# Performance work log

Measured on AMD Instinct MI355X. Metric: run time of the kernel, lower is better.

The kernel has to match this reference:

```python
import jax, jax.numpy as jnp
import numpy as np

N_NODES = 50000


def _gcn_norm(edge_index, edge_weight, num_nodes):
    """Add self-loops (weight 1) and compute symmetric GCN normalization.
    Returns (src, dst, norm) over the augmented edge set."""
    src = jnp.concatenate([edge_index[0], jnp.arange(num_nodes, dtype=edge_index.dtype)])
    dst = jnp.concatenate([edge_index[1], jnp.arange(num_nodes, dtype=edge_index.dtype)])
    w = jnp.concatenate([edge_weight, jnp.ones((num_nodes,), dtype=edge_weight.dtype)])
    deg = jax.ops.segment_sum(w, dst, num_segments=num_nodes)  # [N]
    deg_inv_sqrt = jnp.where(deg > 0, jax.lax.rsqrt(jnp.where(deg > 0, deg, 1.0)), 0.0)
    norm = deg_inv_sqrt[src] * w * deg_inv_sqrt[dst]  # [E+N]
    return src, dst, norm


def _gcn_conv(x, W, b, src, dst, norm, num_nodes):
    h = x @ W                                   # [N, out] linear first (PyG order)
    msg = h[src] * norm[:, None]                # [E+N, out] gather + scale
    out = jax.ops.segment_sum(msg, dst, num_segments=num_nodes)  # scatter-add
    return out + b


def setup_inputs() -> dict:
    key = jax.random.key(0)
    ks = jax.random.split(key, 9)
    N, E = N_NODES, 800000
    x = jax.random.normal(ks[0], (N, 256), dtype=jnp.float32)
    edge_index = jax.random.randint(ks[1], (2, E), 0, N, dtype=jnp.int64)
    edge_attr = jax.random.uniform(ks[2], (E,), dtype=jnp.float32)
    W1 = jax.random.normal(ks[3], (256, 128), dtype=jnp.float32) * (1.0 / np.sqrt(256))
    b1 = jnp.zeros((128,), dtype=jnp.float32)
    W2 = jax.random.normal(ks[4], (128, 128), dtype=jnp.float32) * (1.0 / np.sqrt(128))
    b2 = jnp.zeros((128,), dtype=jnp.float32)
    W3 = jax.random.normal(ks[5], (128, 128), dtype=jnp.float32) * (1.0 / np.sqrt(128))
    b3 = jnp.zeros((128,), dtype=jnp.float32)
    return {"x": x, "edge_index": edge_index, "edge_attr": edge_attr,
            "W1": W1, "b1": b1, "W2": W2, "b2": b2, "W3": W3, "b3": b3}


def reference(x, edge_index, edge_attr, W1, b1, W2, b2, W3, b3):
    N = x.shape[0]
    src, dst, norm = _gcn_norm(edge_index, edge_attr, N)
    x1 = jax.nn.relu(_gcn_conv(x, W1, b1, src, dst, norm, N))
    x2 = jax.nn.relu(_gcn_conv(x1, W2, b2, src, dst, norm, N))
    return jax.nn.relu(_gcn_conv(x2, W3, b3, src, dst, norm, N))
```

## Files before the change

kernel.cpp:

```cpp
#include <hip/hip_runtime.h>
#include <math.h>

#define F_OUT 128
#define MAXDEG 64

typedef __attribute__((ext_vector_type(8))) short short8v;
typedef __attribute__((ext_vector_type(4))) float f32x4;
typedef unsigned long long ull;

__device__ inline ushort f2bf(float x) {
    uint u = __float_as_uint(x);
    uint r = (u + 0x7FFFu + ((u >> 16) & 1u)) >> 16;
    return (ushort)r;
}
__device__ inline float bf2f(ushort h) { return __uint_as_float((uint)h << 16); }
__device__ inline uint pack2(ushort a, ushort b) { return (uint)a | ((uint)b << 16); }

__device__ inline float slot_sumw(ull s) {
    return (float)((double)(s & ((1ull << 40) - 1)) * (1.0 / 8388608.0));
}


__global__ __launch_bounds__(128) void prep_kernel(const float* __restrict__ W1,
                                                   ushort* W1th, ushort* W1tl,
                                                   ull* slot, int n) {
    int b = blockIdx.x;
    if (b < 256) {
        int idx = b * 128 + threadIdx.x;
        int k = idx >> 7, c = idx & 127;
        float x = W1[idx];
        ushort h = f2bf(x);
        ushort l = f2bf(x - bf2f(h));
        W1th[(size_t)c * 256 + k] = h;
        W1tl[(size_t)c * 256 + k] = l;
    } else {
        int i = (b - 256) * 128 + threadIdx.x;
        if (i < n) slot[i] = 0ull;
    }
}


__device__ __forceinline__ void fill_edge(const int* __restrict__ src,
                                          const int* __restrict__ dst,
                                          const float* __restrict__ w,
                                          ull* slot, int2* es, int e) {
    int s = src[e], d = dst[e];
    float wv = w[e];
    ull inc = (1ull << 40) | (ull)(uint)(wv * 8388608.0f + 0.5f);
    ull old = atomicAdd(&slot[d], inc);
    uint pos = (uint)(old >> 40);
    if (pos < MAXDEG) es[(size_t)d * MAXDEG + pos] = make_int2(s, __float_as_int(wv));
}

__global__ void coef_kernel(int2* es, const ull* __restrict__ slot, int n) {
    int i = blockIdx.x * blockDim.x + threadIdx.x;
    if (i < n * MAXDEG) {
        int d = i >> 6;
        int pos = i & (MAXDEG - 1);
        int cnt = (int)(slot[d] >> 40);
        if (pos < cnt) {
            int2 e = es[i];
            float dsrc = rsqrtf(1.0f + slot_sumw(slot[e.x]));
            es[i].y = __float_as_int(dsrc * __int_as_float(e.y));
        }
    }
}


template <int K>
__device__ __forceinline__ void gemm_body(ushort* sAh, ushort* sAl,
                                          ushort* sBh, ushort* sBl,
                                          const float* __restrict__ in,
                                          const ushort* __restrict__ Wth,
                                          const ushort* __restrict__ Wtl,
                                          ushort* __restrict__ hbf, int n, int bb) {
    const int t = threadIdx.x;
    const int lane = t & 63;
    const int wv = t >> 6;
    const int block_row = bb * 64;

    const int arow = t >> 1;
    const int ahalf = t & 1;
    const int bcol = t;

    const int l15 = lane & 15;
    const int koct = lane >> 4;

    f32x4 acc[4][4];
    #pragma unroll
    for (int r = 0; r < 4; ++r)
        #pragma unroll
        for (int c = 0; c < 4; ++c) acc[r][c] = (f32x4){0.f, 0.f, 0.f, 0.f};

    const int grow_a = block_row + arow;
    const bool arow_ok = grow_a < n;

    for (int kt = 0; kt < K / 32; ++kt) {
        const int k0 = kt * 32;

        {
            float v[16];
            if (arow_ok) {
                const float4* p = reinterpret_cast<const float4*>(
                    &in[(size_t)grow_a * K + k0 + ahalf * 16]);
                float4 f0 = p[0], f1 = p[1], f2 = p[2], f3 = p[3];
                v[0]=f0.x; v[1]=f0.y; v[2]=f0.z; v[3]=f0.w;
                v[4]=f1.x; v[5]=f1.y; v[6]=f1.z; v[7]=f1.w;
                v[8]=f2.x; v[9]=f2.y; v[10]=f2.z; v[11]=f2.w;
                v[12]=f3.x; v[13]=f3.y; v[14]=f3.z; v[15]=f3.w;
            } else {
                #pragma unroll
                for (int i = 0; i < 16; ++i) v[i] = 0.f;
            }
            ushort hh[16], ll[16];
            #pragma unroll
            for (int i = 0; i < 16; ++i) {
                hh[i] = f2bf(v[i]);
                ll[i] = f2bf(v[i] - bf2f(hh[i]));
            }
            const int c0 = 2 * ahalf, c1 = 2 * ahalf + 1;
            *reinterpret_cast<uint4*>(&sAh[(c0 * 64 + arow) * 8]) =
                make_uint4(pack2(hh[0],hh[1]), pack2(hh[2],hh[3]), pack2(hh[4],hh[5]), pack2(hh[6],hh[7]));
            *reinterpret_cast<uint4*>(&sAh[(c1 * 64 + arow) * 8]) =
                make_uint4(pack2(hh[8],hh[9]), pack2(hh[10],hh[11]), pack2(hh[12],hh[13]), pack2(hh[14],hh[15]));
            *reinterpret_cast<uint4*>(&sAl[(c0 * 64 + arow) * 8]) =
                make_uint4(pack2(ll[0],ll[1]), pack2(ll[2],ll[3]), pack2(ll[4],ll[5]), pack2(ll[6],ll[7]));
            *reinterpret_cast<uint4*>(&sAl[(c1 * 64 + arow) * 8]) =
                make_uint4(pack2(ll[8],ll[9]), pack2(ll[10],ll[11]), pack2(ll[12],ll[13]), pack2(ll[14],ll[15]));
        }
        {
            const uint4* ph = reinterpret_cast<const uint4*>(&Wth[(size_t)bcol * K + k0]);
            const uint4* pl = reinterpret_cast<const uint4*>(&Wtl[(size_t)bcol * K + k0]);
            #pragma unroll
            for (int j = 0; j < 4; ++j)
                *reinterpret_cast<uint4*>(&sBh[(j * 128 + bcol) * 8]) = ph[j];
            #pragma unroll
            for (int j = 0; j < 4; ++j)
                *reinterpret_cast<uint4*>(&sBl[(j * 128 + bcol) * 8]) = pl[j];
        }
        __syncthreads();

        short8v a_h[4], a_l[4], b_h[4], b_l[4];
        #pragma unroll
        for (int r = 0; r < 4; ++r) {
            a_h[r] = *reinterpret_cast<const short8v*>(&sAh[(koct * 64 + r * 16 + l15) * 8]);
            a_l[r] = *reinterpret_cast<const short8v*>(&sAl[(koct * 64 + r * 16 + l15) * 8]);
        }
        #pragma unroll
        for (int c = 0; c < 4; ++c) {
            b_h[c] = *reinterpret_cast<const short8v*>(&sBh[(koct * 128 + wv * 64 + c * 16 + l15) * 8]);
            b_l[c] = *reinterpret_cast<const short8v*>(&sBl[(koct * 128 + wv * 64 + c * 16 + l15) * 8]);
        }
        #pragma unroll
        for (int r = 0; r < 4; ++r)
            #pragma unroll
            for (int c = 0; c < 4; ++c) {
                acc[r][c] = __builtin_amdgcn_mfma_f32_16x16x32_bf16(a_h[r], b_h[c], acc[r][c], 0, 0, 0);
                acc[r][c] = __builtin_amdgcn_mfma_f32_16x16x32_bf16(a_h[r], b_l[c], acc[r][c], 0, 0, 0);
                acc[r][c] = __builtin_amdgcn_mfma_f32_16x16x32_bf16(a_l[r], b_h[c], acc[r][c], 0, 0, 0);
            }
        __syncthreads();
    }

    #pragma unroll
    for (int r = 0; r < 4; ++r) {
        #pragma unroll
        for (int c = 0; c < 4; ++c) {
            int gcol = wv * 64 + c * 16 + l15;
            #pragma unroll
            for (int j = 0; j < 4; ++j) {
                int grow = block_row + r * 16 + koct * 4 + j;
                if (grow < n) hbf[(size_t)grow * F_OUT + gcol] = f2bf(acc[r][c][j]);
            }
        }
    }
}


template <int K>
__global__ __launch_bounds__(128) void gemm_presplit(const ushort* __restrict__ ahp,
                                                     const ushort* __restrict__ alp,
                                                     const ushort* __restrict__ Wth,
                                                     const ushort* __restrict__ Wtl,
                                                     ushort* __restrict__ hbf, int n) {
    __shared__ ushort sAh[64 * 32], sAl[64 * 32];
    __shared__ ushort sBh[128 * 32], sBl[128 * 32];

    const int t = threadIdx.x;
    const int lane = t & 63;
    const int wv = t >> 6;
    const int block_row = blockIdx.x * 64;

    const int arow = t >> 1;
    const int ahalf = t & 1;
    const int bcol = t;

    const int l15 = lane & 15;
    const int koct = lane >> 4;

    f32x4 acc[4][4];
    #pragma unroll
    for (int r = 0; r < 4; ++r)
        #pragma unroll
        for (int c = 0; c < 4; ++c) acc[r][c] = (f32x4){0.f, 0.f, 0.f, 0.f};

    const int grow_a = block_row + arow;
    const bool arow_ok = grow_a < n;
    const uint4 zero4 = make_uint4(0u, 0u, 0u, 0u);

    for (int kt = 0; kt < K / 32; ++kt) {
        const int k0 = kt * 32;
        const int c0 = 2 * ahalf, c1 = 2 * ahalf + 1;

        if (arow_ok) {
            const uint4* ph = reinterpret_cast<const uint4*>(&ahp[(size_t)grow_a * K + k0 + ahalf * 16]);
            const uint4* pl = reinterpret_cast<const uint4*>(&alp[(size_t)grow_a * K + k0 + ahalf * 16]);
            *reinterpret_cast<uint4*>(&sAh[(c0 * 64 + arow) * 8]) = ph[0];
            *reinterpret_cast<uint4*>(&sAh[(c1 * 64 + arow) * 8]) = ph[1];
            *reinterpret_cast<uint4*>(&sAl[(c0 * 64 + arow) * 8]) = pl[0];
            *reinterpret_cast<uint4*>(&sAl[(c1 * 64 + arow) * 8]) = pl[1];
        } else {
            *reinterpret_cast<uint4*>(&sAh[(c0 * 64 + arow) * 8]) = zero4;
            *reinterpret_cast<uint4*>(&sAh[(c1 * 64 + arow) * 8]) = zero4;
            *reinterpret_cast<uint4*>(&sAl[(c0 * 64 + arow) * 8]) = zero4;
            *reinterpret_cast<uint4*>(&sAl[(c1 * 64 + arow) * 8]) = zero4;
        }
        {
            const uint4* ph = reinterpret_cast<const uint4*>(&Wth[(size_t)bcol * K + k0]);
            const uint4* pl = reinterpret_cast<const uint4*>(&Wtl[(size_t)bcol * K + k0]);
            #pragma unroll
            for (int j = 0; j < 4; ++j)
                *reinterpret_cast<uint4*>(&sBh[(j * 128 + bcol) * 8]) = ph[j];
            #pragma unroll
            for (int j = 0; j < 4; ++j)
                *reinterpret_cast<uint4*>(&sBl[(j * 128 + bcol) * 8]) = pl[j];
        }
        __syncthreads();

        short8v a_h[4], a_l[4], b_h[4], b_l[4];
        #pragma unroll
        for (int r = 0; r < 4; ++r) {
            a_h[r] = *reinterpret_cast<const short8v*>(&sAh[(koct * 64 + r * 16 + l15) * 8]);
            a_l[r] = *reinterpret_cast<const short8v*>(&sAl[(koct * 64 + r * 16 + l15) * 8]);
        }
        #pragma unroll
        for (int c = 0; c < 4; ++c) {
            b_h[c] = *reinterpret_cast<const short8v*>(&sBh[(koct * 128 + wv * 64 + c * 16 + l15) * 8]);
            b_l[c] = *reinterpret_cast<const short8v*>(&sBl[(koct * 128 + wv * 64 + c * 16 + l15) * 8]);
        }
        #pragma unroll
        for (int r = 0; r < 4; ++r)
            #pragma unroll
            for (int c = 0; c < 4; ++c) {
                acc[r][c] = __builtin_amdgcn_mfma_f32_16x16x32_bf16(a_h[r], b_h[c], acc[r][c], 0, 0, 0);
                acc[r][c] = __builtin_amdgcn_mfma_f32_16x16x32_bf16(a_h[r], b_l[c], acc[r][c], 0, 0, 0);
                acc[r][c] = __builtin_amdgcn_mfma_f32_16x16x32_bf16(a_l[r], b_h[c], acc[r][c], 0, 0, 0);
            }
        __syncthreads();
    }

    #pragma unroll
    for (int r = 0; r < 4; ++r) {
        #pragma unroll
        for (int c = 0; c < 4; ++c) {
            int gcol = wv * 64 + c * 16 + l15;
            #pragma unroll
            for (int j = 0; j < 4; ++j) {
                int grow = block_row + r * 16 + koct * 4 + j;
                if (grow < n) hbf[(size_t)grow * F_OUT + gcol] = f2bf(acc[r][c][j]);
            }
        }
    }
}


__global__ __launch_bounds__(128) void mega1_kernel(
        const float* __restrict__ x,
        const ushort* __restrict__ W1th, const ushort* __restrict__ W1tl,
        ushort* __restrict__ hbf,
        const int* __restrict__ src, const int* __restrict__ dst,
        const float* __restrict__ w, ull* slot, int2* es,
        const float* __restrict__ W2, ushort* W2th, ushort* W2tl,
        const float* __restrict__ W3, ushort* W3th, ushort* W3tl,
        int n, int E, int GB, int FB) {
    __shared__ ushort sAh[64 * 32], sAl[64 * 32];
    __shared__ ushort sBh[128 * 32], sBl[128 * 32];

    int b = blockIdx.x;
    if (b < GB) {
        gemm_body<256>(sAh, sAl, sBh, sBl, x, W1th, W1tl, hbf, n, b);
    } else if (b < GB + FB) {
        int e = (b - GB) * 128 + threadIdx.x;
        if (e < E) fill_edge(src, dst, w, slot, es, e);
    } else {
        int wb = b - GB - FB;
        const float* W = (wb < 128) ? W2 : W3;
        ushort* Th = (wb < 128) ? W2th : W3th;
        ushort* Tl = (wb < 128) ? W2tl : W3tl;
        int idx = (wb & 127) * 128 + threadIdx.x;
        int k = idx >> 7, c = idx & 127;
        float v = W[idx];
        ushort h = f2bf(v);
        ushort l = f2bf(v - bf2f(h));
        Th[(size_t)c * 128 + k] = h;
        Tl[(size_t)c * 128 + k] = l;
    }
}


__device__ __forceinline__ void gacc(uint u, float c, float& ax, float& ay) {
    ax += c * __uint_as_float(u << 16);
    ay += c * __uint_as_float(u & 0xFFFF0000u);
}

template <bool SPLIT_OUT>
__global__ __launch_bounds__(256) void gather_kernel(const ushort* __restrict__ hbf,
                                                     const int2* __restrict__ es,
                                                     const ull* __restrict__ slot,
                                                     const float* __restrict__ bias,
                                                     ushort* __restrict__ oah,
                                                     ushort* __restrict__ oal,
                                                     float* __restrict__ outf, int n) {
    int wave = threadIdx.x >> 6;
    int lane = threadIdx.x & 63;
    int node = blockIdx.x * 4 + wave;
    if (node >= n) return;

    int f = lane * 2;
    ull sl = slot[node];
    int cnt = (int)(sl >> 40);
    if (cnt > MAXDEG) cnt = MAXDEG;
    float dd = rsqrtf(1.0f + slot_sumw(sl));

    uint hv = *reinterpret_cast<const uint*>(&hbf[(size_t)node * F_OUT + f]);
    float accx = dd * __uint_as_float(hv << 16);
    float accy = dd * __uint_as_float(hv & 0xFFFF0000u);

    const int2* ep = es + (size_t)node * MAXDEG;
    int i = 0;
    for (; i + 15 < cnt; i += 16) {
        int4 p[8];
        #pragma unroll
        for (int q = 0; q < 8; ++q) p[q] = *reinterpret_cast<const int4*>(&ep[i + 2 * q]);
        uint u[16];
        #pragma unroll
        for (int q = 0; q < 8; ++q) {
            u[2 * q]     = *reinterpret_cast<const uint*>(&hbf[(size_t)p[q].x * F_OUT + f]);
            u[2 * q + 1] = *reinterpret_cast<const uint*>(&hbf[(size_t)p[q].z * F_OUT + f]);
        }
        #pragma unroll
        for (int q = 0; q < 8; ++q) {
            gacc(u[2 * q],     __int_as_float(p[q].y), accx, accy);
            gacc(u[2 * q + 1], __int_as_float(p[q].w), accx, accy);
        }
    }
    for (; i + 7 < cnt; i += 8) {
        int4 p01 = *reinterpret_cast<const int4*>(&ep[i]);
        int4 p23 = *reinterpret_cast<const int4*>(&ep[i + 2]);
        int4 p45 = *reinterpret_cast<const int4*>(&ep[i + 4]);
        int4 p67 = *reinterpret_cast<const int4*>(&ep[i + 6]);
        uint u0 = *reinterpret_cast<const uint*>(&hbf[(size_t)p01.x * F_OUT + f]);
        uint u1 = *reinterpret_cast<const uint*>(&hbf[(size_t)p01.z * F_OUT + f]);
        uint u2 = *reinterpret_cast<const uint*>(&hbf[(size_t)p23.x * F_OUT + f]);
        uint u3 = *reinterpret_cast<const uint*>(&hbf[(size_t)p23.z * F_OUT + f]);
        uint u4 = *reinterpret_cast<const uint*>(&hbf[(size_t)p45.x * F_OUT + f]);
        uint u5 = *reinterpret_cast<const uint*>(&hbf[(size_t)p45.z * F_OUT + f]);
        uint u6 = *reinterpret_cast<const uint*>(&hbf[(size_t)p67.x * F_OUT + f]);
        uint u7 = *reinterpret_cast<const uint*>(&hbf[(size_t)p67.z * F_OUT + f]);
        gacc(u0, __int_as_float(p01.y), accx, accy);
        gacc(u1, __int_as_float(p01.w), accx, accy);
        gacc(u2, __int_as_float(p23.y), accx, accy);
        gacc(u3, __int_as_float(p23.w), accx, accy);
        gacc(u4, __int_as_float(p45.y), accx, accy);
        gacc(u5, __int_as_float(p45.w), accx, accy);
        gacc(u6, __int_as_float(p67.y), accx, accy);
        gacc(u7, __int_as_float(p67.w), accx, accy);
    }
    for (; i + 1 < cnt; i += 2) {
        int4 p01 = *reinterpret_cast<const int4*>(&ep[i]);
        uint u0 = *reinterpret_cast<const uint*>(&hbf[(size_t)p01.x * F_OUT + f]);
        uint u1 = *reinterpret_cast<const uint*>(&hbf[(size_t)p01.z * F_OUT + f]);
        gacc(u0, __int_as_float(p01.y), accx, accy);
        gacc(u1, __int_as_float(p01.w), accx, accy);
    }
    if (i < cnt) {
        int2 e0 = ep[i];
        uint u0 = *reinterpret_cast<const uint*>(&hbf[(size_t)e0.x * F_OUT + f]);
        gacc(u0, __int_as_float(e0.y), accx, accy);
    }

    float rx = fmaxf(bias[f]     + dd * accx, 0.f);
    float ry = fmaxf(bias[f + 1] + dd * accy, 0.f);

    if (SPLIT_OUT) {
        ushort hx = f2bf(rx), hy = f2bf(ry);
        ushort lx = f2bf(rx - bf2f(hx)), ly = f2bf(ry - bf2f(hy));
        *reinterpret_cast<uint*>(&oah[(size_t)node * F_OUT + f]) = pack2(hx, hy);
        *reinterpret_cast<uint*>(&oal[(size_t)node * F_OUT + f]) = pack2(lx, ly);
    } else {
        *reinterpret_cast<float2*>(&outf[(size_t)node * F_OUT + f]) = make_float2(rx, ry);
    }
}


extern "C" void kernel_launch(void* const* d_in, const int* in_sizes, int n_in,
                              void* d_out, int out_size, void* d_ws, size_t ws_size,
                              hipStream_t stream) {
    const float* x  = (const float*)d_in[0];
    const int*   ei = (const int*)  d_in[1];
    const float* ew = (const float*)d_in[2];
    const float* W1 = (const float*)d_in[3];
    const float* b1 = (const float*)d_in[4];
    const float* W2 = (const float*)d_in[5];
    const float* b2 = (const float*)d_in[6];
    const float* W3 = (const float*)d_in[7];
    const float* b3 = (const float*)d_in[8];
    float* out = (float*)d_out;

    const int E = in_sizes[2];
    const int n = in_sizes[0] / 256;
    const int* src = ei;
    const int* dst = ei + E;

    char* ws = (char*)d_ws;
    ull*   slot  = (ull*)ws;
    int2*  es    = (int2*)(slot + n);
    ushort* hbf  = (ushort*)(es + (size_t)n * MAXDEG);
    ushort* aah  = hbf + (size_t)n * F_OUT;
    ushort* aal  = aah + (size_t)n * F_OUT;
    ushort* W1th = aal + (size_t)n * F_OUT;
    ushort* W1tl = W1th + 128 * 256;
    ushort* W2th = W1tl + 128 * 256;
    ushort* W2tl = W2th + 128 * 128;
    ushort* W3th = W2tl + 128 * 128;
    ushort* W3tl = W3th + 128 * 128;

    const int GB = (n + 63) / 64;
    const int FB = (E + 127) / 128;
    const int prep_grid = 256 + (n + 127) / 128;

    prep_kernel<<<prep_grid, 128, 0, stream>>>(W1, W1th, W1tl, slot, n);

    mega1_kernel<<<GB + FB + 256, 128, 0, stream>>>(
        x, W1th, W1tl, hbf, src, dst, ew, slot, es,
        W2, W2th, W2tl, W3, W3th, W3tl, n, E, GB, FB);

    coef_kernel<<<(n * MAXDEG + 255) / 256, 256, 0, stream>>>(es, slot, n);

    const int gather_grid = (n + 3) / 4;

    gather_kernel<true><<<gather_grid, 256, 0, stream>>>(hbf, es, slot, b1, aah, aal, nullptr, n);

    gemm_presplit<128><<<GB, 128, 0, stream>>>(aah, aal, W2th, W2tl, hbf, n);
    gather_kernel<true><<<gather_grid, 256, 0, stream>>>(hbf, es, slot, b2, aah, aal, nullptr, n);

    gemm_presplit<128><<<GB, 128, 0, stream>>>(aah, aal, W3th, W3tl, hbf, n);
    gather_kernel<false><<<gather_grid, 256, 0, stream>>>(hbf, es, slot, b3, nullptr, nullptr, out, n);
}
```

Before: 208.3 us.

## Fuse neighbor gather with next layer GEMM via shared-memory staged activations

Each gather and the following 128x128 GEMM become one kernel. A block gathers 64 nodes, splits them into bf16 hi/lo in shared memory and multiplies by the next weight matrix there. This drops the global round trip of the split activations (aah/aal) and two kernel launches, and uses ping-pong hbf buffers instead. In exchange, each wave gathers 16 nodes one after another, giving fewer independent gathers in flight per block and less latency hiding than the one-node-per-wave gather.

```diff
diff --git a/kernel.cpp b/kernel.cpp
--- a/kernel.cpp
+++ b/kernel.cpp
@@ -67,6 +67,78 @@
 }
 
 
+__device__ __forceinline__ void gacc(uint u, float c, float& ax, float& ay) {
+    ax += c * __uint_as_float(u << 16);
+    ay += c * __uint_as_float(u & 0xFFFF0000u);
+}
+
+__device__ __forceinline__ float2 gather_node(const ushort* __restrict__ hin,
+                                              const int2* __restrict__ ep,
+                                              int cnt, float dd, int node, int f,
+                                              float bx, float by) {
+    uint hv = *reinterpret_cast<const uint*>(&hin[(size_t)node * F_OUT + f]);
+    float accx = dd * __uint_as_float(hv << 16);
+    float accy = dd * __uint_as_float(hv & 0xFFFF0000u);
+
+    int i = 0;
+    for (; i + 15 < cnt; i += 16) {
+        int4 p[8];
+        #pragma unroll
+        for (int q = 0; q < 8; ++q) p[q] = *reinterpret_cast<const int4*>(&ep[i + 2 * q]);
+        uint u[16];
+        #pragma unroll
+        for (int q = 0; q < 8; ++q) {
+            u[2 * q]     = *reinterpret_cast<const uint*>(&hin[(size_t)p[q].x * F_OUT + f]);
+            u[2 * q + 1] = *reinterpret_cast<const uint*>(&hin[(size_t)p[q].z * F_OUT + f]);
+        }
+        #pragma unroll
+        for (int q = 0; q < 8; ++q) {
+            gacc(u[2 * q],     __int_as_float(p[q].y), accx, accy);
+            gacc(u[2 * q + 1], __int_as_float(p[q].w), accx, accy);
+        }
+    }
+    for (; i + 7 < cnt; i += 8) {
+        int4 p01 = *reinterpret_cast<const int4*>(&ep[i]);
+        int4 p23 = *reinterpret_cast<const int4*>(&ep[i + 2]);
+        int4 p45 = *reinterpret_cast<const int4*>(&ep[i + 4]);
+        int4 p67 = *reinterpret_cast<const int4*>(&ep[i + 6]);
+        uint u0 = *reinterpret_cast<const uint*>(&hin[(size_t)p01.x * F_OUT + f]);
+        uint u1 = *reinterpret_cast<const uint*>(&hin[(size_t)p01.z * F_OUT + f]);
+        uint u2 = *reinterpret_cast<const uint*>(&hin[(size_t)p23.x * F_OUT + f]);
+        uint u3 = *reinterpret_cast<const uint*>(&hin[(size_t)p23.z * F_OUT + f]);
+        uint u4 = *reinterpret_cast<const uint*>(&hin[(size_t)p45.x * F_OUT + f]);
+        uint u5 = *reinterpret_cast<const uint*>(&hin[(size_t)p45.z * F_OUT + f]);
+        uint u6 = *reinterpret_cast<const uint*>(&hin[(size_t)p67.x * F_OUT + f]);
+        uint u7 = *reinterpret_cast<const uint*>(&hin[(size_t)p67.z * F_OUT + f]);
+        gacc(u0, __int_as_float(p01.y), accx, accy);
+        gacc(u1, __int_as_float(p01.w), accx, accy);
+        gacc(u2, __int_as_float(p23.y), accx, accy);
+        gacc(u3, __int_as_float(p23.w), accx, accy);
+        gacc(u4, __int_as_float(p45.y), accx, accy);
+        gacc(u5, __int_as_float(p45.w), accx, accy);
+        gacc(u6, __int_as_float(p67.y), accx, accy);
+        gacc(u7, __int_as_float(p67.w), accx, accy);
+    }
+    for (; i + 1 < cnt; i += 2) {
+        int4 p01 = *reinterpret_cast<const int4*>(&ep[i]);
+        uint u0 = *reinterpret_cast<const uint*>(&hin[(size_t)p01.x * F_OUT + f]);
+        uint u1 = *reinterpret_cast<const uint*>(&hin[(size_t)p01.z * F_OUT + f]);
+        gacc(u0, __int_as_float(p01.y), accx, accy);
+        gacc(u1, __int_as_float(p01.w), accx, accy);
+    }
+    if (i < cnt) {
+        int2 e0 = ep[i];
+        uint u0 = *reinterpret_cast<const uint*>(&hin[(size_t)e0.x * F_OUT + f]);
+        gacc(u0, __int_as_float(e0.y), accx, accy);
+    }
+
+    float2 r;
+    r.x = fmaxf(bx + dd * accx, 0.f);
+    r.y = fmaxf(by + dd * accy, 0.f);
+    return r;
+}
+
+
 template <int K>
 __device__ __forceinline__ void gemm_body(ushort* sAh, ushort* sAl,
                                           ushort* sBh, ushort* sBl,
@@ -127,103 +199,6 @@
                 make_uint4(pack2(ll[0],ll[1]), pack2(ll[2],ll[3]), pack2(ll[4],ll[5]), pack2(ll[6],ll[7]));
             *reinterpret_cast<uint4*>(&sAl[(c1 * 64 + arow) * 8]) =
                 make_uint4(pack2(ll[8],ll[9]), pack2(ll[10],ll[11]), pack2(ll[12],ll[13]), pack2(ll[14],ll[15]));
-        }
-        {
-            const uint4* ph = reinterpret_cast<const uint4*>(&Wth[(size_t)bcol * K + k0]);
-            const uint4* pl = reinterpret_cast<const uint4*>(&Wtl[(size_t)bcol * K + k0]);
-            #pragma unroll
-            for (int j = 0; j < 4; ++j)
-                *reinterpret_cast<uint4*>(&sBh[(j * 128 + bcol) * 8]) = ph[j];
-            #pragma unroll
-            for (int j = 0; j < 4; ++j)
-                *reinterpret_cast<uint4*>(&sBl[(j * 128 + bcol) * 8]) = pl[j];
-        }
-        __syncthreads();
-
-        short8v a_h[4], a_l[4], b_h[4], b_l[4];
-        #pragma unroll
-        for (int r = 0; r < 4; ++r) {
-            a_h[r] = *reinterpret_cast<const short8v*>(&sAh[(koct * 64 + r * 16 + l15) * 8]);
-            a_l[r] = *reinterpret_cast<const short8v*>(&sAl[(koct * 64 + r * 16 + l15) * 8]);
-        }
-        #pragma unroll
-        for (int c = 0; c < 4; ++c) {
-            b_h[c] = *reinterpret_cast<const short8v*>(&sBh[(koct * 128 + wv * 64 + c * 16 + l15) * 8]);
-            b_l[c] = *reinterpret_cast<const short8v*>(&sBl[(koct * 128 + wv * 64 + c * 16 + l15) * 8]);
-        }
-        #pragma unroll
-        for (int r = 0; r < 4; ++r)
-            #pragma unroll
-            for (int c = 0; c < 4; ++c) {
-                acc[r][c] = __builtin_amdgcn_mfma_f32_16x16x32_bf16(a_h[r], b_h[c], acc[r][c], 0, 0, 0);
-                acc[r][c] = __builtin_amdgcn_mfma_f32_16x16x32_bf16(a_h[r], b_l[c], acc[r][c], 0, 0, 0);
-                acc[r][c] = __builtin_amdgcn_mfma_f32_16x16x32_bf16(a_l[r], b_h[c], acc[r][c], 0, 0, 0);
-            }
-        __syncthreads();
-    }
-
-    #pragma unroll
-    for (int r = 0; r < 4; ++r) {
-        #pragma unroll
-        for (int c = 0; c < 4; ++c) {
-            int gcol = wv * 64 + c * 16 + l15;
-            #pragma unroll
-            for (int j = 0; j < 4; ++j) {
-                int grow = block_row + r * 16 + koct * 4 + j;
-                if (grow < n) hbf[(size_t)grow * F_OUT + gcol] = f2bf(acc[r][c][j]);
-            }
-        }
-    }
-}
-
-
-template <int K>
-__global__ __launch_bounds__(128) void gemm_presplit(const ushort* __restrict__ ahp,
-                                                     const ushort* __restrict__ alp,
-                                                     const ushort* __restrict__ Wth,
-                                                     const ushort* __restrict__ Wtl,
-                                                     ushort* __restrict__ hbf, int n) {
-    __shared__ ushort sAh[64 * 32], sAl[64 * 32];
-    __shared__ ushort sBh[128 * 32], sBl[128 * 32];
-
-    const int t = threadIdx.x;
-    const int lane = t & 63;
-    const int wv = t >> 6;
-    const int block_row = blockIdx.x * 64;
-
-    const int arow = t >> 1;
-    const int ahalf = t & 1;
-    const int bcol = t;
-
-    const int l15 = lane & 15;
-    const int koct = lane >> 4;
-
-    f32x4 acc[4][4];
-    #pragma unroll
-    for (int r = 0; r < 4; ++r)
-        #pragma unroll
-        for (int c = 0; c < 4; ++c) acc[r][c] = (f32x4){0.f, 0.f, 0.f, 0.f};
-
-    const int grow_a = block_row + arow;
-    const bool arow_ok = grow_a < n;
-    const uint4 zero4 = make_uint4(0u, 0u, 0u, 0u);
-
-    for (int kt = 0; kt < K / 32; ++kt) {
-        const int k0 = kt * 32;
-        const int c0 = 2 * ahalf, c1 = 2 * ahalf + 1;
-
-        if (arow_ok) {
-            const uint4* ph = reinterpret_cast<const uint4*>(&ahp[(size_t)grow_a * K + k0 + ahalf * 16]);
-            const uint4* pl = reinterpret_cast<const uint4*>(&alp[(size_t)grow_a * K + k0 + ahalf * 16]);
-            *reinterpret_cast<uint4*>(&sAh[(c0 * 64 + arow) * 8]) = ph[0];
-            *reinterpret_cast<uint4*>(&sAh[(c1 * 64 + arow) * 8]) = ph[1];
-            *reinterpret_cast<uint4*>(&sAl[(c0 * 64 + arow) * 8]) = pl[0];
-            *reinterpret_cast<uint4*>(&sAl[(c1 * 64 + arow) * 8]) = pl[1];
-        } else {
-            *reinterpret_cast<uint4*>(&sAh[(c0 * 64 + arow) * 8]) = zero4;
-            *reinterpret_cast<uint4*>(&sAh[(c1 * 64 + arow) * 8]) = zero4;
-            *reinterpret_cast<uint4*>(&sAl[(c0 * 64 + arow) * 8]) = zero4;
-            *reinterpret_cast<uint4*>(&sAl[(c1 * 64 + arow) * 8]) = zero4;
         }
         {
             const uint4* ph = reinterpret_cast<const uint4*>(&Wth[(size_t)bcol * K + k0]);
@@ -308,19 +283,114 @@
 }
 
 
-__device__ __forceinline__ void gacc(uint u, float c, float& ax, float& ay) {
-    ax += c * __uint_as_float(u << 16);
-    ay += c * __uint_as_float(u & 0xFFFF0000u);
-}
-
-template <bool SPLIT_OUT>
-__global__ __launch_bounds__(256) void gather_kernel(const ushort* __restrict__ hbf,
-                                                     const int2* __restrict__ es,
-                                                     const ull* __restrict__ slot,
-                                                     const float* __restrict__ bias,
-                                                     ushort* __restrict__ oah,
-                                                     ushort* __restrict__ oal,
-                                                     float* __restrict__ outf, int n) {
+#define AROWS 65
+
+__global__ __launch_bounds__(256) void fused_gg(
+        const ushort* __restrict__ hin,
+        const int2* __restrict__ es,
+        const ull* __restrict__ slot,
+        const float* __restrict__ bias,
+        const ushort* __restrict__ Wth, const ushort* __restrict__ Wtl,
+        ushort* __restrict__ hout, int n) {
+    __shared__ ushort sAh[16 * AROWS * 8], sAl[16 * AROWS * 8];
+    __shared__ ushort sBh[4 * 128 * 8],    sBl[4 * 128 * 8];
+
+    const int t = threadIdx.x;
+    const int wv = t >> 6;
+    const int lane = t & 63;
+    const int block_row = blockIdx.x * 64;
+    const int f = lane * 2;
+
+    {
+        const float bx = bias[f], by = bias[f + 1];
+        const int chunk = f >> 3;
+        const int fo = f & 7;
+        for (int it = 0; it < 16; ++it) {
+            int nl = wv * 16 + it;
+            int node = block_row + nl;
+            float2 r = make_float2(0.f, 0.f);
+            if (node < n) {
+                ull sl = slot[node];
+                int cnt = (int)(sl >> 40);
+                if (cnt > MAXDEG) cnt = MAXDEG;
+                float dd = rsqrtf(1.0f + slot_sumw(sl));
+                r = gather_node(hin, es + (size_t)node * MAXDEG, cnt, dd, node, f, bx, by);
+            }
+            ushort hx = f2bf(r.x), hy = f2bf(r.y);
+            ushort lx = f2bf(r.x - bf2f(hx)), ly = f2bf(r.y - bf2f(hy));
+            int off = (chunk * AROWS + nl) * 8 + fo;
+            *reinterpret_cast<uint*>(&sAh[off]) = pack2(hx, hy);
+            *reinterpret_cast<uint*>(&sAl[off]) = pack2(lx, ly);
+        }
+    }
+    __syncthreads();
+
+    const int l15 = lane & 15;
+    const int koct = lane >> 4;
+    f32x4 acc[4][2];
+    #pragma unroll
+    for (int r = 0; r < 4; ++r)
+        #pragma unroll
+        for (int c = 0; c < 2; ++c) acc[r][c] = (f32x4){0.f, 0.f, 0.f, 0.f};
+
+    const int bcol = t & 127;
+    const int jh = (t >> 7) * 2;
+
+    for (int kt = 0; kt < 4; ++kt) {
+        {
+            const uint4* ph = reinterpret_cast<const uint4*>(&Wth[(size_t)bcol * 128 + kt * 32 + jh * 8]);
+            const uint4* pl = reinterpret_cast<const uint4*>(&Wtl[(size_t)bcol * 128 + kt * 32 + jh * 8]);
+            *reinterpret_cast<uint4*>(&sBh[(jh * 128 + bcol) * 8])       = ph[0];
+            *reinterpret_cast<uint4*>(&sBh[((jh + 1) * 128 + bcol) * 8]) = ph[1];
+            *reinterpret_cast<uint4*>(&sBl[(jh * 128 + bcol) * 8])       = pl[0];
+            *reinterpret_cast<uint4*>(&sBl[((jh + 1) * 128 + bcol) * 8]) = pl[1];
+        }
+        __syncthreads();
+
+        short8v a_h[4], a_l[4], b_h[2], b_l[2];
+        #pragma unroll
+        for (int r = 0; r < 4; ++r) {
+            int off = (((kt * 4 + koct) * AROWS) + r * 16 + l15) * 8;
+            a_h[r] = *reinterpret_cast<const short8v*>(&sAh[off]);
+            a_l[r] = *reinterpret_cast<const short8v*>(&sAl[off]);
+        }
+        #pragma unroll
+        for (int c = 0; c < 2; ++c) {
+            int off = (koct * 128 + wv * 32 + c * 16 + l15) * 8;
+            b_h[c] = *reinterpret_cast<const short8v*>(&sBh[off]);
+            b_l[c] = *reinterpret_cast<const short8v*>(&sBl[off]);
+        }
+        #pragma unroll
+        for (int r = 0; r < 4; ++r)
+            #pragma unroll
+            for (int c = 0; c < 2; ++c) {
+                acc[r][c] = __builtin_amdgcn_mfma_f32_16x16x32_bf16(a_h[r], b_h[c], acc[r][c], 0, 0, 0);
+                acc[r][c] = __builtin_amdgcn_mfma_f32_16x16x32_bf16(a_h[r], b_l[c], acc[r][c], 0, 0, 0);
+                acc[r][c] = __builtin_amdgcn_mfma_f32_16x16x32_bf16(a_l[r], b_h[c], acc[r][c], 0, 0, 0);
+            }
+        __syncthreads();
+    }
+
+    #pragma unroll
+    for (int r = 0; r < 4; ++r) {
+        #pragma unroll
+        for (int c = 0; c < 2; ++c) {
+            int gcol = wv * 32 + c * 16 + l15;
+            #pragma unroll
+            for (int j = 0; j < 4; ++j) {
+                int grow = block_row + r * 16 + koct * 4 + j;
+                if (grow < n) hout[(size_t)grow * F_OUT + gcol] = f2bf(acc[r][c][j]);
+            }
+        }
+    }
+}
+
+
+__global__ __launch_bounds__(256) void gather_final(const ushort* __restrict__ hbf,
+                                                    const int2* __restrict__ es,
+                                                    const ull* __restrict__ slot,
+                                                    const float* __restrict__ bias,
+                                                    float* __restrict__ outf, int n) {
     int wave = threadIdx.x >> 6;
     int lane = threadIdx.x & 63;
     int node = blockIdx.x * 4 + wave;
@@ -332,74 +402,9 @@
     if (cnt > MAXDEG) cnt = MAXDEG;
     float dd = rsqrtf(1.0f + slot_sumw(sl));
 
-    uint hv = *reinterpret_cast<const uint*>(&hbf[(size_t)node * F_OUT + f]);
-    float accx = dd * __uint_as_float(hv << 16);
-    float accy = dd * __uint_as_float(hv & 0xFFFF0000u);
-
-    const int2* ep = es + (size_t)node * MAXDEG;
-    int i = 0;
-    for (; i + 15 < cnt; i += 16) {
-        int4 p[8];
-        #pragma unroll
-        for (int q = 0; q < 8; ++q) p[q] = *reinterpret_cast<const int4*>(&ep[i + 2 * q]);
-        uint u[16];
-        #pragma unroll
-        for (int q = 0; q < 8; ++q) {
-            u[2 * q]     = *reinterpret_cast<const uint*>(&hbf[(size_t)p[q].x * F_OUT + f]);
-            u[2 * q + 1] = *reinterpret_cast<const uint*>(&hbf[(size_t)p[q].z * F_OUT + f]);
-        }
-        #pragma unroll
-        for (int q = 0; q < 8; ++q) {
-            gacc(u[2 * q],     __int_as_float(p[q].y), accx, accy);
-            gacc(u[2 * q + 1], __int_as_float(p[q].w), accx, accy);
-        }
-    }
-    for (; i + 7 < cnt; i += 8) {
-        int4 p01 = *reinterpret_cast<const int4*>(&ep[i]);
-        int4 p23 = *reinterpret_cast<const int4*>(&ep[i + 2]);
-        int4 p45 = *reinterpret_cast<const int4*>(&ep[i + 4]);
-        int4 p67 = *reinterpret_cast<const int4*>(&ep[i + 6]);
-        uint u0 = *reinterpret_cast<const uint*>(&hbf[(size_t)p01.x * F_OUT + f]);
-        uint u1 = *reinterpret_cast<const uint*>(&hbf[(size_t)p01.z * F_OUT + f]);
-        uint u2 = *reinterpret_cast<const uint*>(&hbf[(size_t)p23.x * F_OUT + f]);
-        uint u3 = *reinterpret_cast<const uint*>(&hbf[(size_t)p23.z * F_OUT + f]);
-        uint u4 = *reinterpret_cast<const uint*>(&hbf[(size_t)p45.x * F_OUT + f]);
-        uint u5 = *reinterpret_cast<const uint*>(&hbf[(size_t)p45.z * F_OUT + f]);
-        uint u6 = *reinterpret_cast<const uint*>(&hbf[(size_t)p67.x * F_OUT + f]);
-        uint u7 = *reinterpret_cast<const uint*>(&hbf[(size_t)p67.z * F_OUT + f]);
-        gacc(u0, __int_as_float(p01.y), accx, accy);
-        gacc(u1, __int_as_float(p01.w), accx, accy);
-        gacc(u2, __int_as_float(p23.y), accx, accy);
-        gacc(u3, __int_as_float(p23.w), accx, accy);
-        gacc(u4, __int_as_float(p45.y), accx, accy);
-        gacc(u5, __int_as_float(p45.w), accx, accy);
-        gacc(u6, __int_as_float(p67.y), accx, accy);
-        gacc(u7, __int_as_float(p67.w), accx, accy);
-    }
-    for (; i + 1 < cnt; i += 2) {
-        int4 p01 = *reinterpret_cast<const int4*>(&ep[i]);
-        uint u0 = *reinterpret_cast<const uint*>(&hbf[(size_t)p01.x * F_OUT + f]);
-        uint u1 = *reinterpret_cast<const uint*>(&hbf[(size_t)p01.z * F_OUT + f]);
-        gacc(u0, __int_as_float(p01.y), accx, accy);
-        gacc(u1, __int_as_float(p01.w), accx, accy);
-    }
-    if (i < cnt) {
-        int2 e0 = ep[i];
-        uint u0 = *reinterpret_cast<const uint*>(&hbf[(size_t)e0.x * F_OUT + f]);
-        gacc(u0, __int_as_float(e0.y), accx, accy);
-    }
-
-    float rx = fmaxf(bias[f]     + dd * accx, 0.f);
-    float ry = fmaxf(bias[f + 1] + dd * accy, 0.f);
-
-    if (SPLIT_OUT) {
-        ushort hx = f2bf(rx), hy = f2bf(ry);
-        ushort lx = f2bf(rx - bf2f(hx)), ly = f2bf(ry - bf2f(hy));
-        *reinterpret_cast<uint*>(&oah[(size_t)node * F_OUT + f]) = pack2(hx, hy);
-        *reinterpret_cast<uint*>(&oal[(size_t)node * F_OUT + f]) = pack2(lx, ly);
-    } else {
-        *reinterpret_cast<float2*>(&outf[(size_t)node * F_OUT + f]) = make_float2(rx, ry);
-    }
+    float2 r = gather_node(hbf, es + (size_t)node * MAXDEG, cnt, dd, node, f,
+                           bias[f], bias[f + 1]);
+    *reinterpret_cast<float2*>(&outf[(size_t)node * F_OUT + f]) = r;
 }
 
 
@@ -425,10 +430,9 @@
     char* ws = (char*)d_ws;
     ull*   slot  = (ull*)ws;
     int2*  es    = (int2*)(slot + n);
-    ushort* hbf  = (ushort*)(es + (size_t)n * MAXDEG);
-    ushort* aah  = hbf + (size_t)n * F_OUT;
-    ushort* aal  = aah + (size_t)n * F_OUT;
-    ushort* W1th = aal + (size_t)n * F_OUT;
+    ushort* hbfA = (ushort*)(es + (size_t)n * MAXDEG);
+    ushort* hbfB = hbfA + (size_t)n * F_OUT;
+    ushort* W1th = hbfB + (size_t)n * F_OUT;
     ushort* W1tl = W1th + 128 * 256;
     ushort* W2th = W1tl + 128 * 256;
     ushort* W2tl = W2th + 128 * 128;
@@ -442,18 +446,14 @@
     prep_kernel<<<prep_grid, 128, 0, stream>>>(W1, W1th, W1tl, slot, n);
 
     mega1_kernel<<<GB + FB + 256, 128, 0, stream>>>(
-        x, W1th, W1tl, hbf, src, dst, ew, slot, es,
+        x, W1th, W1tl, hbfA, src, dst, ew, slot, es,
         W2, W2th, W2tl, W3, W3th, W3tl, n, E, GB, FB);
 
     coef_kernel<<<(n * MAXDEG + 255) / 256, 256, 0, stream>>>(es, slot, n);
 
-    const int gather_grid = (n + 3) / 4;
-
-    gather_kernel<true><<<gather_grid, 256, 0, stream>>>(hbf, es, slot, b1, aah, aal, nullptr, n);
-
-    gemm_presplit<128><<<GB, 128, 0, stream>>>(aah, aal, W2th, W2tl, hbf, n);
-    gather_kernel<true><<<gather_grid, 256, 0, stream>>>(hbf, es, slot, b2, aah, aal, nullptr, n);
-
-    gemm_presplit<128><<<GB, 128, 0, stream>>>(aah, aal, W3th, W3tl, hbf, n);
-    gather_kernel<false><<<gather_grid, 256, 0, stream>>>(hbf, es, slot, b3, nullptr, nullptr, out, n);
-}
+    fused_gg<<<GB, 256, 0, stream>>>(hbfA, es, slot, b1, W2th, W2tl, hbfB, n);
+
+    fused_gg<<<GB, 256, 0, stream>>>(hbfB, es, slot, b2, W3th, W3tl, hbfA, n);
+
+    gather_final<<<(n + 3) / 4, 256, 0, stream>>>(hbfA, es, slot, b3, out, n);
+}
```

New measurement: 295.0 us. 1.42x slower.
